# Kernel tuning notes

Hardware: AMD Instinct MI355X
Metric: run time of the kernel (lower is better)

## Reference

```python
import jax, jax.numpy as jnp
import numpy as np

EPS = 1e-5
GRID = 24          # GRID_SIZE
IMG = 96           # IMAGE_SIZE[0]
SCALE = IMG / GRID # 4.0
X0, X1 = -112.0, 224.0
Y0, Y1 = 0.0, 224.0
CIN = 48
CMID = 24
NKP = 4
B = 1024


def _conv(x, w):
    # x: [B,C,H,W], w: [O,I,kh,kw]
    return jax.lax.conv_general_dilated(x, w, (1, 1), 'SAME',
                                        dimension_numbers=('NCHW', 'OIHW', 'NCHW'))


def _head(x, w1, b1, g, be, m, v, w2, b2, sig):
    y = _conv(x, w1) + b1[None, :, None, None]
    inv = jax.lax.rsqrt(v + EPS)
    y = (y - m[None, :, None, None]) * (g * inv)[None, :, None, None] + be[None, :, None, None]
    y = jax.nn.relu(y)
    y = _conv(y, w2) + b2[None, :, None, None]
    return jax.nn.sigmoid(y) if sig else y


def _head_params(key, cout):
    ks = jax.random.split(key, 4)
    w1 = jax.random.normal(ks[0], (CMID, CIN, 3, 3), jnp.float32) * 0.05
    b1 = jnp.zeros((CMID,), jnp.float32)
    g = jnp.ones((CMID,), jnp.float32)
    be = jnp.zeros((CMID,), jnp.float32)
    m = jax.random.normal(ks[1], (CMID,), jnp.float32) * 0.1
    v = jax.random.uniform(ks[2], (CMID,), jnp.float32, 0.5, 1.5)
    w2 = jax.random.normal(ks[3], (cout, CMID, 1, 1), jnp.float32) * 0.05
    b2 = jnp.zeros((cout,), jnp.float32)
    return w1, b1, g, be, m, v, w2, b2


def setup_inputs() -> dict:
    key = jax.random.key(0)
    k0, kc, kk, kr, ko = jax.random.split(key, 5)
    d = {'features': jax.random.normal(k0, (B, CIN * GRID * GRID), jnp.float32)}
    for pref, kk_, cout in (('c', kc, 1), ('k', kk, NKP), ('r', kr, 2 * NKP), ('o', ko, 2 * NKP)):
        w1, b1, g, be, m, v, w2, b2 = _head_params(kk_, cout)
        d[pref + 'w1'], d[pref + 'b1'] = w1, b1
        d[pref + 'g'], d[pref + 'be'] = g, be
        d[pref + 'm'], d[pref + 'v'] = m, v
        d[pref + 'w2'], d[pref + 'b2'] = w2, b2
    return d


def reference(features,
              cw1, cb1, cg, cbe, cm, cv, cw2, cb2,
              kw1, kb1, kg, kbe, km, kv, kw2, kb2,
              rw1, rb1, rg, rbe, rm, rv, rw2, rb2,
              ow1, ob1, og, obe, om, ov, ow2, ob2):
    Bn = features.shape[0]
    x = features.reshape(Bn, CIN, GRID, GRID)
    center = _head(x, cw1, cb1, cg, cbe, cm, cv, cw2, cb2, True)    # [B,1,H,W]
    kp = _head(x, kw1, kb1, kg, kbe, km, kv, kw2, kb2, True)        # [B,N,H,W]
    reg = _head(x, rw1, rb1, rg, rbe, rm, rv, rw2, rb2, False)      # [B,2N,H,W]
    off = _head(x, ow1, ob1, og, obe, om, ov, ow2, ob2, False)      # [B,2N,H,W]

    H = W = GRID
    hm = kp.reshape(Bn, NKP, H * W)
    idx = jnp.argmax(hm, axis=2)                                   # [B,N]
    my = (idx // W).astype(jnp.float32)
    mx = (idx % W).astype(jnp.float32)
    # offset channels: (n*2) -> x, (n*2+1) -> y
    off_r = off.reshape(Bn, NKP, 2, H * W)
    g = jnp.take_along_axis(off_r, idx[:, :, None, None], axis=3)[..., 0]  # [B,N,2]
    ox, oy = g[..., 0], g[..., 1]
    fx = (mx + ox) * SCALE + X0
    fy = (my + oy) * SCALE + Y0
    pix = jnp.stack([fx, fy], axis=-1).reshape(Bn, 2 * NKP)        # [B,8]
    norm = jnp.stack([(fx - X0) / (X1 - X0), (fy - Y0) / (Y1 - Y0)], axis=-1).reshape(Bn, 2 * NKP)
    return (center, kp, reg, off, norm, pix)
```

## Files before the change

### kernel.cpp

```cpp
#include <hip/hip_runtime.h>
#include <stdint.h>

#define HW    576
#define CIN   48
#define NB    1024

#define O_CENTER 0L
#define O_KP     589824L
#define O_REG    2949120L
#define O_OFF    7667712L
#define O_NORM   12386304L
#define O_PIX    12394496L

#define WS_A1    0
#define WS_W2A   82944
#define WS_B1A   89088
#define WS_B2A   89472
#define WS_WKPT  89600
#define WS_B1KP  131072
#define WS_W2KP  131168
#define WS_B2KP  131552
#define WS_WOFFT 131584
#define WS_B1OFF 173056
#define WS_W2OFF 173152
#define WS_B2OFF 174688

typedef short bf16x8 __attribute__((ext_vector_type(8)));
typedef float f32x16 __attribute__((ext_vector_type(16)));

union U4B  { uint4 q; bf16x8 v; };
union U16Q { uint16_t u[8]; uint4 q; };
union U4Q  { uint16_t u[4]; uint2 q; };

__device__ __forceinline__ bf16x8 as_bf(uint4 q){ U4B u; u.q = q; return u.v; }
__device__ __forceinline__ uint16_t f2b(float f){
  union { float f; uint32_t i; } x; x.f = f;
  uint32_t r = x.i + 0x7FFFu + ((x.i >> 16) & 1u);
  return (uint16_t)(r >> 16);
}

struct P32 {
  const float* w1[4]; const float* b1[4]; const float* g[4]; const float* be[4];
  const float* m[4];  const float* v[4];  const float* w2[4]; const float* b2[4];
};

__device__ __forceinline__ void oc_decode(int oc, int& h, int& ch){
  if (oc == 0){ h = 0; ch = 0; }
  else if (oc < 5){ h = 1; ch = oc - 1; }
  else if (oc < 13){ h = 2; ch = oc - 5; }
  else { h = 3; ch = oc - 13; }
}

__global__ void prep_kernel(P32 P, char* __restrict__ wsb){
  const int tid = threadIdx.x;
  __shared__ float sc[96], bfold[96];
  if (tid < 96){
    int h = tid / 24, o = tid % 24;
    float s = P.g[h][o] / sqrtf(P.v[h][o] + 1e-5f);
    sc[tid] = s;
    bfold[tid] = (P.b1[h][o] - P.m[h][o]) * s + P.be[h][o];
  }
  __syncthreads();
  uint16_t* A1 = (uint16_t*)(wsb + WS_A1);
  for (int t = tid; t < 41472; t += 256){
    int j = t & 7, slot = t >> 3;
    int row = slot % 96, sk = slot / 96;
    int g = sk & 1, k3 = (sk >> 1) % 3, sh = (sk >> 1) / 3;
    int ci = k3*16 + g*8 + j;
    int h = row / 24, o = row % 24;
    A1[t] = f2b(P.w1[h][(o*CIN + ci)*9 + sh] * sc[row]);
  }
  uint16_t* W2A = (uint16_t*)(wsb + WS_W2A);
  for (int t = tid; t < 3072; t += 256){
    int j = t & 7, slot = t >> 3;
    int oc = slot & 31, kg = slot >> 5;
    int k = kg*8 + j;
    float val = 0.f;
    if (oc < 21){
      int h, ch; oc_decode(oc, h, ch);
      int hk = k / 24, o = k % 24;
      if (hk == h) val = P.w2[h][ch*24 + o];
    }
    W2A[t] = f2b(val);
  }
  float* B1A = (float*)(wsb + WS_B1A);
  if (tid < 96) B1A[tid] = bfold[tid];
  float* B2A = (float*)(wsb + WS_B2A);
  if (tid < 32){
    float v = 0.f;
    if (tid < 21){ int h, ch; oc_decode(tid, h, ch); v = P.b2[h][ch]; }
    B2A[tid] = v;
  }
  float* WKPT = (float*)(wsb + WS_WKPT);
  for (int t = tid; t < 10368; t += 256){
    int o = t % 24, k = (t/24) % 9, ci = t / 216;
    WKPT[t] = P.w1[1][(o*CIN + ci)*9 + k] * sc[24 + o];
  }
  if (tid < 24) ((float*)(wsb + WS_B1KP))[tid] = bfold[24 + tid];
  if (tid < 96) ((float*)(wsb + WS_W2KP))[tid] = P.w2[1][tid];
  if (tid < 4)  ((float*)(wsb + WS_B2KP))[tid] = P.b2[1][tid];
  float* WOFFT = (float*)(wsb + WS_WOFFT);
  for (int t = tid; t < 10368; t += 256){
    int o = t / 432;
    WOFFT[t] = P.w1[3][t] * sc[72 + o];
  }
  if (tid < 24)  ((float*)(wsb + WS_B1OFF))[tid] = bfold[72 + tid];
  for (int t = tid; t < 384; t += 256) ((float*)(wsb + WS_W2OFF))[t] = P.w2[3][t];
  if (tid < 16)  ((float*)(wsb + WS_B2OFF))[tid] = P.b2[3][tid];
}

__global__ __launch_bounds__(576) void conv_main(
    const float* __restrict__ feat, const char* __restrict__ wsb,
    float* __restrict__ out)
{
  __shared__ __align__(16) char smem[60000];
  const int b = blockIdx.x, tid = threadIdx.x;
  const int wave = tid >> 6, lane = tid & 63;
  const int q = lane >> 5, l31 = lane & 31;

  if (tid < 294){
    int cib = tid / 49, r = tid % 49;
    int slot = cib*625 + ((r < 25) ? r : (r - 24)*25);
    *(uint4*)(smem + slot*16) = make_uint4(0,0,0,0);
  }
  {
    const float* fb = feat + (size_t)b * (CIN*HW);
    int p = tid, py = p / 24, px = p % 24;
    int sbase = (py+1)*25 + (px+1);
    for (int cib = 0; cib < 6; ++cib){
      U16Q t8;
      #pragma unroll
      for (int j = 0; j < 8; ++j) t8.u[j] = f2b(fb[(cib*8 + j)*HW + p]);
      *(uint4*)(smem + (cib*625 + sbase)*16) = t8.q;
    }
  }
  __syncthreads();

  f32x16 acc[3][2] = {};
  const int p0 = wave*64 + l31, p1 = p0 + 32;
  const int py0 = p0/24, px0 = p0%24, py1 = p1/24, px1 = p1%24;
  const uint4* A1 = (const uint4*)(wsb + WS_A1);
  const uint4 zz = make_uint4(0,0,0,0);

  for (int sh = 0; sh < 9; ++sh){
    const int ky = sh / 3, kx = sh % 3;
    const int yb0 = py0 + ky, xb0 = px0 + kx;
    const int yb1 = py1 + ky, xb1 = px1 + kx;
    const bool v0 = (yb0 < 25) && (xb0 < 25);
    const bool v1 = (yb1 < 25) && (xb1 < 25);
    const int so0 = yb0*25 + xb0, so1 = yb1*25 + xb1;
    #pragma unroll
    for (int k3 = 0; k3 < 3; ++k3){
      const int cib = k3*2 + q;
      uint4 r0 = *(const uint4*)(smem + (cib*625 + (v0 ? so0 : 0))*16);
      uint4 r1 = *(const uint4*)(smem + (cib*625 + (v1 ? so1 : 0))*16);
      r0 = v0 ? r0 : zz;
      r1 = v1 ? r1 : zz;
      const bf16x8 bf0 = as_bf(r0), bf1 = as_bf(r1);
      const int abase = ((sh*3 + k3)*2 + q)*96 + l31;
      #pragma unroll
      for (int mt = 0; mt < 3; ++mt){
        const bf16x8 af = as_bf(A1[abase + mt*32]);
        acc[mt][0] = __builtin_amdgcn_mfma_f32_32x32x16_bf16(af, bf0, acc[mt][0], 0, 0, 0);
        acc[mt][1] = __builtin_amdgcn_mfma_f32_32x32x16_bf16(af, bf1, acc[mt][1], 0, 0, 0);
      }
    }
  }
  __syncthreads();

  const float* B1A = (const float*)(wsb + WS_B1A);
  const float* B2A = (const float*)(wsb + WS_B2A);
  const uint4* W2A = (const uint4*)(wsb + WS_W2A);
  char* ybuf = smem + wave*6144;

  #pragma unroll
  for (int st2 = 0; st2 < 2; ++st2){
    const int p = st2 ? p1 : p0;
    #pragma unroll
    for (int mt = 0; mt < 3; ++mt){
      #pragma unroll
      for (int rg = 0; rg < 4; ++rg){
        const int chanbase = mt*32 + rg*8 + q*4;
        const float* bp = B1A + chanbase;
        U4Q t4;
        #pragma unroll
        for (int r0 = 0; r0 < 4; ++r0){
          float y = acc[mt][st2][rg*4 + r0] + bp[r0];
          t4.u[r0] = f2b(fmaxf(y, 0.f));
        }
        *(uint2*)(ybuf + ((mt*4 + rg)*32 + l31)*16 + q*8) = t4.q;
      }
    }
    f32x16 c2 = {};
    #pragma unroll
    for (int k6 = 0; k6 < 6; ++k6){
      const bf16x8 yf = as_bf(*(const uint4*)(ybuf + ((k6*2 + q)*32 + l31)*16));
      const bf16x8 wf = as_bf(W2A[(k6*2 + q)*32 + l31]);
      c2 = __builtin_amdgcn_mfma_f32_32x32x16_bf16(wf, yf, c2, 0, 0, 0);
    }
    #pragma unroll
    for (int r = 0; r < 16; ++r){
      const int oc = (r & 3) + 8*(r >> 2) + 4*q;
      if (oc < 21){
        float v = c2[r] + B2A[oc];
        long base; int sig;
        if (oc == 0){ base = O_CENTER + (long)b*HW; sig = 1; }
        else if (oc < 5){ base = O_KP + ((long)b*4 + (oc-1))*HW; sig = 1; }
        else if (oc < 13){ base = O_REG + ((long)b*8 + (oc-5))*HW; sig = 0; }
        else { base = O_OFF + ((long)b*8 + (oc-13))*HW; sig = 0; }
        out[base + p] = sig ? (1.f / (1.f + __expf(-v))) : v;
      }
    }
  }
}

__global__ __launch_bounds__(576) void kp_select(
    const float* __restrict__ feat, const char* __restrict__ wsb,
    float* __restrict__ out)
{
  __shared__ __align__(16) float simg[8*26*24];
  __shared__ float wk_lds[8*9*24];
  __shared__ float ykp [96*24];
  __shared__ __align__(16) float opatch[4][432];
  __shared__ float ymidL[4*24];
  __shared__ int   jobL[4*HW];
  __shared__ int   KtotL;
  __shared__ unsigned long long bestL[4];

  const int b = blockIdx.x, tid = threadIdx.x;
  if (tid == 0) KtotL = 0;
  if (tid < 4) bestL[tid] = 0ULL;
  __syncthreads();

  if (tid < 256){
    const int n = tid >> 6, ln = tid & 63;
    const float* sp = out + O_KP + ((long)b*4 + n)*HW;
    float s[9];
    #pragma unroll
    for (int j = 0; j < 9; ++j) s[j] = sp[j*64 + ln];
    float mx = s[0];
    #pragma unroll
    for (int j = 1; j < 9; ++j) mx = fmaxf(mx, s[j]);
    #pragma unroll
    for (int off = 32; off >= 1; off >>= 1)
      mx = fmaxf(mx, __shfl_xor(mx, off, 64));
    const float sm = fminf(mx, 0.999999f);
    const float thr = sm / (sm + (1.f - sm) * 1.1331485f);
    #pragma unroll
    for (int j = 0; j < 9; ++j){
      if (s[j] >= thr){
        const int slot = atomicAdd(&KtotL, 1);
        jobL[slot] = (n << 16) | (j*64 + ln);
      }
    }
  }
  __syncthreads();
  const int Ktot = KtotL;

  const int s24 = tid / 24, omid = tid - s24*24;
  const int dst = (s24 + 1)*24 + omid;
  const float* fb = feat + (size_t)b * (CIN*HW);
  const float* WKPT = (const float*)(wsb + WS_WKPT);
  const float b1k = ((const float*)(wsb + WS_B1KP))[omid];

  for (int g0 = 0; g0 < Ktot; g0 += 96){
    const int Kg = min(96, Ktot - g0);

    int pyc[4], pxc[4];
    #pragma unroll
    for (int c = 0; c < 4; ++c){
      int p = 0;
      if (c*24 + s24 < Kg) p = jobL[g0 + c*24 + s24] & 0xFFFF;
      pyc[c] = p / 24; pxc[c] = p - (p/24)*24;
    }

    float acck[4] = {0.f,0.f,0.f,0.f};

    for (int pass = 0; pass < 6; ++pass){
      __syncthreads();
      if (tid < 384){
        int c = tid / 48, r = tid - c*48;
        int row = (r < 24) ? 0 : 25;
        int col = (r < 24) ? r : r - 24;
        simg[c*624 + row*24 + col] = 0.f;
      }
      #pragma unroll
      for (int c = 0; c < 8; ++c)
        simg[c*624 + dst] = fb[(pass*8 + c)*HW + tid];
      #pragma unroll
      for (int j = 0; j < 3; ++j)
        wk_lds[tid + j*576] = WKPT[pass*1728 + tid + j*576];
      __syncthreads();

      for (int c8 = 0; c8 < 8; ++c8){
        float pch[4][9];
        #pragma unroll
        for (int c = 0; c < 4; ++c) if (c*24 < Kg){
          const int a = c8*624 + pyc[c]*24 + pxc[c];
          const bool wl = (pxc[c] > 0), wr = (pxc[c] < 23);
          #pragma unroll
          for (int dr = 0; dr < 3; ++dr){
            const int aa = a + dr*24;
            pch[c][dr*3+0] = wl ? simg[aa-1] : 0.f;
            pch[c][dr*3+1] = simg[aa];
            pch[c][dr*3+2] = wr ? simg[aa+1] : 0.f;
          }
        }
        const float* wkb = wk_lds + c8*216 + omid;
        #pragma unroll
        for (int k = 0; k < 9; ++k){
          const float wk = wkb[k*24];
          #pragma unroll
          for (int c = 0; c < 4; ++c) if (c*24 < Kg)
            acck[c] = fmaf(pch[c][k], wk, acck[c]);
        }
      }
    }

    #pragma unroll
    for (int c = 0; c < 4; ++c) if (c*24 < Kg){
      const int sl = c*24 + s24;
      ykp[sl*24 + omid] = fmaxf(acck[c] + b1k, 0.f);
    }
    __syncthreads();

    if (tid < Kg){
      const int cand = g0 + tid;
      const int job = jobL[cand];
      const int n = job >> 16, p = job & 0xFFFF;
      const float* W2KP = (const float*)(wsb + WS_W2KP);
      float v = ((const float*)(wsb + WS_B2KP))[n];
      #pragma unroll
      for (int o = 0; o < 24; ++o)
        v = fmaf(ykp[tid*24 + o], W2KP[n*24 + o], v);
      union { float f; uint32_t u; } cv; cv.f = v;
      const uint32_t key = cv.u ^ (uint32_t)(((int32_t)cv.u >> 31) | (int32_t)0x80000000);
      const unsigned long long pk =
          ((unsigned long long)key << 32) | (unsigned)(1023 - p);
      atomicMax(&bestL[n], pk);
    }
    __syncthreads();
  }

  #pragma unroll
  for (int j = 0; j < 3; ++j){
    const int e = tid*3 + j;
    const int w = e / 432, idx = e - w*432;
    const int ci = idx / 9, k = idx - ci*9;
    const int p = 1023 - (int)(bestL[w] & 0xFFFFFFFFu);
    const int py = p / 24, px = p % 24;
    const int yy = py + k/3 - 1, xx = px + (k - (k/3)*3) - 1;
    float v = 0.f;
    if (yy >= 0 && yy < 24 && xx >= 0 && xx < 24)
      v = fb[ci*HW + yy*24 + xx];
    opatch[w][idx] = v;
  }
  __syncthreads();

  if (tid < 96){
    const int n = tid / 24, mid = tid - n*24;
    const float* wrow = (const float*)(wsb + WS_WOFFT) + mid*432;
    const float* prow = opatch[n];
    float s = 0.f;
    #pragma unroll 4
    for (int t = 0; t < 108; ++t){
      const float4 pv = *(const float4*)(prow + t*4);
      const float4 wv = *(const float4*)(wrow + t*4);
      s = fmaf(pv.x, wv.x, s);
      s = fmaf(pv.y, wv.y, s);
      s = fmaf(pv.z, wv.z, s);
      s = fmaf(pv.w, wv.w, s);
    }
    ymidL[n*24 + mid] = fmaxf(s + ((const float*)(wsb + WS_B1OFF))[mid], 0.f);
  }
  __syncthreads();

  if (tid < 4){
    const int n = tid;
    const int p = 1023 - (int)(bestL[n] & 0xFFFFFFFFu);
    const int py = p / 24, px = p % 24;
    const float* W2OFF = (const float*)(wsb + WS_W2OFF);
    const float* B2OFF = (const float*)(wsb + WS_B2OFF);
    float ox = B2OFF[2*n], oy = B2OFF[2*n + 1];
    #pragma unroll
    for (int o = 0; o < 24; ++o){
      const float ym = ymidL[n*24 + o];
      ox = fmaf(ym, W2OFF[(2*n)*24 + o], ox);
      oy = fmaf(ym, W2OFF[(2*n + 1)*24 + o], oy);
    }
    const float fx = ((float)px + ox) * 4.f - 112.f;
    const float fy = ((float)py + oy) * 4.f;
    out[O_NORM + b*8 + 2*n    ] = (fx + 112.f) * (1.f/336.f);
    out[O_NORM + b*8 + 2*n + 1] = fy * (1.f/224.f);
    out[O_PIX  + b*8 + 2*n    ] = fx;
    out[O_PIX  + b*8 + 2*n + 1] = fy;
  }
}

extern "C" void kernel_launch(void* const* d_in, const int* in_sizes, int n_in,
                              void* d_out, int out_size, void* d_ws, size_t ws_size,
                              hipStream_t stream)
{
  const float* feat = (const float*)d_in[0];
  P32 P;
  for (int h = 0; h < 4; ++h){
    const int base = 1 + h*8;
    P.w1[h] = (const float*)d_in[base+0];
    P.b1[h] = (const float*)d_in[base+1];
    P.g[h]  = (const float*)d_in[base+2];
    P.be[h] = (const float*)d_in[base+3];
    P.m[h]  = (const float*)d_in[base+4];
    P.v[h]  = (const float*)d_in[base+5];
    P.w2[h] = (const float*)d_in[base+6];
    P.b2[h] = (const float*)d_in[base+7];
  }
  char* wsb = (char*)d_ws;
  float* out = (float*)d_out;

  prep_kernel<<<dim3(1),   256, 0, stream>>>(P, wsb);
  conv_main  <<<dim3(NB),  576, 0, stream>>>(feat, wsb, out);
  kp_select  <<<dim3(NB),  576, 0, stream>>>(feat, wsb, out);
}
```

Before: 630.5 us.

## Split conv_main per image into three 8-row segments with halo loads

conv_main now launches a 2D grid with three blocks per image, each covering 8 output rows with 192 threads and a 10-row halo tile in shared memory (about 23 KB instead of 60 KB). Horizontal padding is handled by bounds checks, and the top and bottom halo rows are zero-filled. The aim is higher occupancy and finer-grained scheduling across CUs. The cost is redundant loading of the halo rows and more blocks overall.

```diff
diff --git a/kernel.cpp b/kernel.cpp
--- a/kernel.cpp
+++ b/kernel.cpp
@@ -109,54 +109,56 @@
   if (tid < 16)  ((float*)(wsb + WS_B2OFF))[tid] = P.b2[3][tid];
 }
 
-__global__ __launch_bounds__(576) void conv_main(
+__global__ __launch_bounds__(192) void conv_main(
     const float* __restrict__ feat, const char* __restrict__ wsb,
     float* __restrict__ out)
 {
-  __shared__ __align__(16) char smem[60000];
-  const int b = blockIdx.x, tid = threadIdx.x;
+  __shared__ __align__(16) char smem[23040];
+  const int b = blockIdx.x, seg = blockIdx.y;
+  const int tid = threadIdx.x;
   const int wave = tid >> 6, lane = tid & 63;
   const int q = lane >> 5, l31 = lane & 31;
-
-  if (tid < 294){
-    int cib = tid / 49, r = tid % 49;
-    int slot = cib*625 + ((r < 25) ? r : (r - 24)*25);
-    *(uint4*)(smem + slot*16) = make_uint4(0,0,0,0);
-  }
+  const int row0 = seg * 8;
+
   {
     const float* fb = feat + (size_t)b * (CIN*HW);
-    int p = tid, py = p / 24, px = p % 24;
-    int sbase = (py+1)*25 + (px+1);
-    for (int cib = 0; cib < 6; ++cib){
+    for (int u = tid; u < 1440; u += 192){
+      const int cib = u / 240, s = u - cib*240;
+      const int sr = s / 24, c = s - sr*24;
+      const int g = row0 - 1 + sr;
       U16Q t8;
-      #pragma unroll
-      for (int j = 0; j < 8; ++j) t8.u[j] = f2b(fb[(cib*8 + j)*HW + p]);
-      *(uint4*)(smem + (cib*625 + sbase)*16) = t8.q;
+      if (g >= 0 && g < 24){
+        #pragma unroll
+        for (int j = 0; j < 8; ++j) t8.u[j] = f2b(fb[(cib*8 + j)*HW + g*24 + c]);
+      } else {
+        #pragma unroll
+        for (int j = 0; j < 8; ++j) t8.u[j] = 0;
+      }
+      *(uint4*)(smem + (cib*240 + s)*16) = t8.q;
     }
   }
   __syncthreads();
 
   f32x16 acc[3][2] = {};
   const int p0 = wave*64 + l31, p1 = p0 + 32;
-  const int py0 = p0/24, px0 = p0%24, py1 = p1/24, px1 = p1%24;
+  const int oy0 = p0/24, ox0 = p0%24, oy1 = p1/24, ox1 = p1%24;
   const uint4* A1 = (const uint4*)(wsb + WS_A1);
   const uint4 zz = make_uint4(0,0,0,0);
 
   for (int sh = 0; sh < 9; ++sh){
     const int ky = sh / 3, kx = sh % 3;
-    const int yb0 = py0 + ky, xb0 = px0 + kx;
-    const int yb1 = py1 + ky, xb1 = px1 + kx;
-    const bool v0 = (yb0 < 25) && (xb0 < 25);
-    const bool v1 = (yb1 < 25) && (xb1 < 25);
-    const int so0 = yb0*25 + xb0, so1 = yb1*25 + xb1;
+    const int xx0 = ox0 + kx - 1, xx1 = ox1 + kx - 1;
+    const bool v0 = (xx0 >= 0) && (xx0 < 24);
+    const bool v1 = (xx1 >= 0) && (xx1 < 24);
+    const int so0 = (oy0 + ky)*24 + xx0, so1 = (oy1 + ky)*24 + xx1;
     #pragma unroll
     for (int k3 = 0; k3 < 3; ++k3){
       const int cib = k3*2 + q;
-      uint4 r0 = *(const uint4*)(smem + (cib*625 + (v0 ? so0 : 0))*16);
-      uint4 r1 = *(const uint4*)(smem + (cib*625 + (v1 ? so1 : 0))*16);
-      r0 = v0 ? r0 : zz;
-      r1 = v1 ? r1 : zz;
-      const bf16x8 bf0 = as_bf(r0), bf1 = as_bf(r1);
+      uint4 ra = *(const uint4*)(smem + (cib*240 + (v0 ? so0 : 0))*16);
+      uint4 rb = *(const uint4*)(smem + (cib*240 + (v1 ? so1 : 0))*16);
+      ra = v0 ? ra : zz;
+      rb = v1 ? rb : zz;
+      const bf16x8 bf0 = as_bf(ra), bf1 = as_bf(rb);
       const int abase = ((sh*3 + k3)*2 + q)*96 + l31;
       #pragma unroll
       for (int mt = 0; mt < 3; ++mt){
@@ -176,6 +178,7 @@
   #pragma unroll
   for (int st2 = 0; st2 < 2; ++st2){
     const int p = st2 ? p1 : p0;
+    const int pg = row0*24 + p;
     #pragma unroll
     for (int mt = 0; mt < 3; ++mt){
       #pragma unroll
@@ -208,7 +211,7 @@
         else if (oc < 5){ base = O_KP + ((long)b*4 + (oc-1))*HW; sig = 1; }
         else if (oc < 13){ base = O_REG + ((long)b*8 + (oc-5))*HW; sig = 0; }
         else { base = O_OFF + ((long)b*8 + (oc-13))*HW; sig = 0; }
-        out[base + p] = sig ? (1.f / (1.f + __expf(-v))) : v;
+        out[base + pg] = sig ? (1.f / (1.f + __expf(-v))) : v;
       }
     }
   }
@@ -417,7 +420,7 @@
   char* wsb = (char*)d_ws;
   float* out = (float*)d_out;
 
-  prep_kernel<<<dim3(1),   256, 0, stream>>>(P, wsb);
-  conv_main  <<<dim3(NB),  576, 0, stream>>>(feat, wsb, out);
-  kp_select  <<<dim3(NB),  576, 0, stream>>>(feat, wsb, out);
-}
+  prep_kernel<<<dim3(1),       256, 0, stream>>>(P, wsb);
+  conv_main  <<<dim3(NB, 3),   192, 0, stream>>>(feat, wsb, out);
+  kp_select  <<<dim3(NB),      576, 0, stream>>>(feat, wsb, out);
+}
```

Result: slower. 670.2 us (+6.3%).
